# Kernel optimization log

Hardware: AMD Instinct MI355X
Metric: run time of the kernel (lower is better)

Reference implementation:

```python
import jax, jax.numpy as jnp
import numpy as np

N, E = 10000, 320000
IN_DIM = HID = OUT_DIM = 128
N_HEADS = 16
HEAD_DIM = OUT_DIM // N_HEADS  # 8
EDGE_FEAT_DIM, R_FEAT_DIM = 4, 64
KV_DIM = 2 * IN_DIM + EDGE_FEAT_DIM + R_FEAT_DIM  # 324
LN_EPS = 1e-5


def _layer_norm(x, g, b):
    mu = x.mean(-1, keepdims=True)
    var = ((x - mu) ** 2).mean(-1, keepdims=True)
    return (x - mu) / jnp.sqrt(var + LN_EPS) * g + b


def _mlp(x, W1, b1, g1, be1, W2, b2):
    # Linear -> LayerNorm -> ReLU -> Linear (2-layer MLP with norm=True)
    return jax.nn.relu(_layer_norm(x @ W1 + b1, g1, be1)) @ W2 + b2


def _mlp_params(key, din, dh, dout):
    k1, k2 = jax.random.split(key)
    return (jax.random.normal(k1, (din, dh), jnp.float32) / np.sqrt(din),
            jnp.zeros((dh,), jnp.float32),
            jnp.ones((dh,), jnp.float32),
            jnp.zeros((dh,), jnp.float32),
            jax.random.normal(k2, (dh, dout), jnp.float32) / np.sqrt(dh),
            jnp.zeros((dout,), jnp.float32))


def setup_inputs() -> dict:
    key = jax.random.key(0)
    ks = jax.random.split(key, 9)
    inp = {
        "h": jax.random.normal(ks[0], (N, IN_DIM), jnp.float32),
        "r_feat": jax.random.normal(ks[1], (E, R_FEAT_DIM), jnp.float32),
        "edge_feat": jax.random.normal(ks[2], (E, EDGE_FEAT_DIM), jnp.float32),
        "edge_index": jax.random.randint(ks[3], (2, E), 0, N, jnp.int32),
    }
    for name, (din, dout), k in [("hk", (KV_DIM, OUT_DIM), ks[4]),
                                 ("hv", (KV_DIM, OUT_DIM), ks[5]),
                                 ("hq", (IN_DIM, OUT_DIM), ks[6]),
                                 ("no", (2 * HID, HID), ks[7])]:
        W1, b1, g1, be1, W2, b2 = _mlp_params(k, din, HID, dout)
        inp.update({f"{name}_W1": W1, f"{name}_b1": b1, f"{name}_g1": g1,
                    f"{name}_be1": be1, f"{name}_W2": W2, f"{name}_b2": b2})
    inp["ew_W"] = jax.random.normal(ks[8], (R_FEAT_DIM, 1), jnp.float32) / np.sqrt(R_FEAT_DIM)
    inp["ew_b"] = jnp.zeros((1,), jnp.float32)
    return inp


def reference(h, r_feat, edge_feat, edge_index,
              hk_W1, hk_b1, hk_g1, hk_be1, hk_W2, hk_b2,
              hv_W1, hv_b1, hv_g1, hv_be1, hv_W2, hv_b2,
              hq_W1, hq_b1, hq_g1, hq_be1, hq_W2, hq_b2,
              no_W1, no_b1, no_g1, no_be1, no_W2, no_b2,
              ew_W, ew_b):
    src, dst = edge_index[0], edge_index[1]
    hi, hj = h[dst], h[src]  # [E, IN_DIM] gathers
    # kv_input = cat([edge_feat, r_feat, hi, hj])  (edge_feat prepended)
    kv_input = jnp.concatenate([edge_feat, r_feat, hi, hj], axis=-1)  # [E, KV_DIM]

    k = _mlp(kv_input, hk_W1, hk_b1, hk_g1, hk_be1, hk_W2, hk_b2).reshape(E, N_HEADS, HEAD_DIM)
    v = _mlp(kv_input, hv_W1, hv_b1, hv_g1, hv_be1, hv_W2, hv_b2)  # [E, OUT_DIM]
    e_w = jax.nn.sigmoid(r_feat @ ew_W + ew_b)  # [E, 1] (ew_net_type == 'r')
    v = (v * e_w).reshape(E, N_HEADS, HEAD_DIM)
    q = _mlp(h, hq_W1, hq_b1, hq_g1, hq_be1, hq_W2, hq_b2).reshape(N, N_HEADS, HEAD_DIM)

    # scatter_softmax over edges grouped by dst, per head
    logits = (q[dst] * k).sum(-1) / np.sqrt(HEAD_DIM)  # [E, N_HEADS]
    seg_max = jax.ops.segment_max(logits, dst, num_segments=N)
    ex = jnp.exp(logits - seg_max[dst])
    den = jax.ops.segment_sum(ex, dst, num_segments=N)
    alpha = ex / (den[dst] + 1e-16)  # [E, N_HEADS]

    msg = alpha[..., None] * v  # [E, N_HEADS, HEAD_DIM]
    out = jax.ops.segment_sum(msg, dst, num_segments=N).reshape(N, OUT_DIM)
    out = _mlp(jnp.concatenate([out, h], axis=-1), no_W1, no_b1, no_g1, no_be1, no_W2, no_b2)
    return out + h
```

## Files before the change

kernel.cpp:

```cpp
#include <hip/hip_runtime.h>
#include <hip/hip_bf16.h>

#define N_NODES 10000
#define N_EDGES 320000

typedef __attribute__((ext_vector_type(8))) short bf16x8;
typedef __attribute__((ext_vector_type(4))) float f32x4;

__device__ inline short f2bf(float x) {
    __hip_bfloat16 h = __float2bfloat16(x);
    union { __hip_bfloat16 h; short s; } u; u.h = h; return u.s;
}

__device__ inline void st_bf4(short* p, float4 v) {
    union { short s[4]; int2 i; } u;
    u.s[0] = f2bf(v.x); u.s[1] = f2bf(v.y); u.s[2] = f2bf(v.z); u.s[3] = f2bf(v.w);
    *(int2*)p = u.i;
}

__device__ inline void block_reduce4(float4& v, float4* red) {
    #pragma unroll
    for (int o = 32; o > 0; o >>= 1) {
        v.x += __shfl_down(v.x, o, 64);
        v.y += __shfl_down(v.y, o, 64);
        v.z += __shfl_down(v.z, o, 64);
        v.w += __shfl_down(v.w, o, 64);
    }
    __syncthreads();
    if ((threadIdx.x & 63) == 0) red[threadIdx.x >> 6] = v;
    __syncthreads();
    float4 a = red[0], b = red[1];
    v.x = a.x + b.x; v.y = a.y + b.y; v.z = a.z + b.z; v.w = a.w + b.w;
}

__global__ __launch_bounds__(256) void prep_wt_kernel(
    const float* __restrict__ Wk, const float* __restrict__ Wv,
    short* __restrict__ Wt, int K)
{
    int col = threadIdx.x, ch = blockIdx.x;
    const float* W = (col < 128) ? Wk : Wv;
    int c = col & 127;
    short tmp[32];
    #pragma unroll
    for (int kk = 0; kk < 32; ++kk) {
        int k = ch * 32 + kk;
        float w = (k < K) ? W[k * 128 + c] : 0.f;
        tmp[kk] = f2bf(w);
    }
    short* outp = Wt + ((size_t)ch * 256 + col) * 32;
    #pragma unroll
    for (int i = 0; i < 4; ++i) {
        union { short s[8]; int4 v; } u;
        #pragma unroll
        for (int j = 0; j < 8; ++j) u.s[j] = tmp[i * 8 + j];
        *(int4*)(outp + i * 8) = u.v;
    }
}

__global__ __launch_bounds__(256) void hist_kernel(
    const int* __restrict__ edge_index, int* __restrict__ cnt)
{
    int stride = gridDim.x * blockDim.x;
    for (int e = blockIdx.x * blockDim.x + threadIdx.x; e < N_EDGES; e += stride)
        atomicAdd(&cnt[edge_index[N_EDGES + e]], 1);
}

__global__ __launch_bounds__(256) void scan_kernel(
    const int* __restrict__ cnt, int* __restrict__ base, int* __restrict__ cursor)
{
    __shared__ int part[256];
    int t = threadIdx.x;
    int lo = t * 40, hi = min(lo + 40, N_NODES);
    int s = 0;
    for (int i = lo; i < hi; ++i) s += cnt[i];
    part[t] = s;
    __syncthreads();
    if (t == 0) {
        int run = 0;
        for (int i = 0; i < 256; ++i) { int v = part[i]; part[i] = run; run += v; }
    }
    __syncthreads();
    int run = part[t];
    for (int i = lo; i < hi; ++i) {
        base[i] = run; cursor[i] = run; run += cnt[i];
    }
}

__global__ __launch_bounds__(256) void scatter_ids_kernel(
    const int* __restrict__ edge_index, int* __restrict__ cursor,
    int* __restrict__ sorted)
{
    int stride = gridDim.x * blockDim.x;
    for (int e = blockIdx.x * blockDim.x + threadIdx.x; e < N_EDGES; e += stride) {
        int d = edge_index[N_EDGES + e];
        int pos = atomicAdd(&cursor[d], 1);
        sorted[pos] = e;
    }
}

__global__ __launch_bounds__(128) void q_kernel(
    const float* __restrict__ h,
    const float* __restrict__ W1, const float* __restrict__ b1,
    const float* __restrict__ g1, const float* __restrict__ be1,
    const float* __restrict__ W2, const float* __restrict__ b2,
    float* __restrict__ qout)
{
    __shared__ __align__(16) float x[128];
    __shared__ __align__(16) float r[128];
    __shared__ float4 red4[2];
    int n = blockIdx.x, tid = threadIdx.x;
    x[tid] = h[(long)n * 128 + tid];
    __syncthreads();
    float y = b1[tid];
    #pragma unroll 4
    for (int i4 = 0; i4 < 128; i4 += 4) {
        float4 c = *(const float4*)&x[i4];
        y = fmaf(c.x, W1[(i4 + 0) * 128 + tid], y);
        y = fmaf(c.y, W1[(i4 + 1) * 128 + tid], y);
        y = fmaf(c.z, W1[(i4 + 2) * 128 + tid], y);
        y = fmaf(c.w, W1[(i4 + 3) * 128 + tid], y);
    }
    float4 s = make_float4(y, y * y, 0.f, 0.f);
    block_reduce4(s, red4);
    float mu  = s.x * 0.0078125f;
    float var = s.y * 0.0078125f - mu * mu;
    float ny = (y - mu) * rsqrtf(var + 1e-5f) * g1[tid] + be1[tid];
    r[tid] = fmaxf(ny, 0.f);
    __syncthreads();
    float y2 = b2[tid];
    #pragma unroll 4
    for (int i4 = 0; i4 < 128; i4 += 4) {
        float4 c = *(const float4*)&r[i4];
        y2 = fmaf(c.x, W2[(i4 + 0) * 128 + tid], y2);
        y2 = fmaf(c.y, W2[(i4 + 1) * 128 + tid], y2);
        y2 = fmaf(c.z, W2[(i4 + 2) * 128 + tid], y2);
        y2 = fmaf(c.w, W2[(i4 + 3) * 128 + tid], y2);
    }
    qout[(long)n * 128 + tid] = y2;
}

__global__ __launch_bounds__(256, 3) void edge_kernel(
    const float* __restrict__ h, const float* __restrict__ r_feat,
    const float* __restrict__ edge_feat, const int* __restrict__ edge_index,
    const short* __restrict__ Wt1, const short* __restrict__ Wt2,
    const float* __restrict__ kb1, const float* __restrict__ kg1,
    const float* __restrict__ kbe1, const float* __restrict__ kb2,
    const float* __restrict__ vb1, const float* __restrict__ vg1,
    const float* __restrict__ vbe1, const float* __restrict__ vb2,
    const float* __restrict__ ewW, const float* __restrict__ ewb,
    const float* __restrict__ q,
    float* __restrict__ logits_g, short* __restrict__ voutS)
{
    __shared__ __align__(16) char smem[53760];
    short* A1   = (short*)smem;
    short* A2   = (short*)smem;
    short* vbuf = (short*)smem;
    float* qbuf = (float*)(smem + 17408);
    float* ln_s = (float*)(smem + 51200);
    float* ln_q = (float*)(smem + 52224);
    float* ew_s = (float*)(smem + 53248);
    int*   dst_s= (int*)(smem + 53504);

    const int tid  = threadIdx.x;
    const int w    = tid >> 6;
    const int lane = tid & 63;
    const int g    = lane >> 4;
    const int lr   = lane & 15;
    const int cw   = w * 64;
    const long eg0 = (long)blockIdx.x * 64;

    {
        int row = tid >> 2;
        int c4  = tid & 3;
        long eg = eg0 + row;
        int srcn = edge_index[eg];
        int dstn = edge_index[N_EDGES + eg];
        if (c4 == 0) dst_s[row] = dstn;
        short* arow = A1 + row * 360;
        if (c4 == 0) {
            float4 v = *(const float4*)&edge_feat[eg * 4];
            st_bf4(arow, v);
        }
        #pragma unroll
        for (int j = 0; j < 4; ++j) {
            float4 v = *(const float4*)&r_feat[eg * 64 + c4 * 16 + j * 4];
            st_bf4(arow + 4 + c4 * 16 + j * 4, v);
        }
        #pragma unroll
        for (int j = 0; j < 8; ++j) {
            float4 v = *(const float4*)&h[(size_t)dstn * 128 + c4 * 32 + j * 4];
            st_bf4(arow + 68 + c4 * 32 + j * 4, v);
        }
        #pragma unroll
        for (int j = 0; j < 8; ++j) {
            float4 v = *(const float4*)&h[(size_t)srcn * 128 + c4 * 32 + j * 4];
            st_bf4(arow + 196 + c4 * 32 + j * 4, v);
        }
        for (int gi = c4; gi < 9; gi += 4)
            *(int2*)(arow + 324 + gi * 4) = make_int2(0, 0);

        float p = 0.f;
        #pragma unroll
        for (int j = 0; j < 4; ++j) {
            float4 rv = *(const float4*)&r_feat[eg * 64 + c4 * 16 + j * 4];
            float4 wv = *(const float4*)&ewW[c4 * 16 + j * 4];
            p += rv.x * wv.x + rv.y * wv.y + rv.z * wv.z + rv.w * wv.w;
        }
        p += __shfl_xor(p, 1);
        p += __shfl_xor(p, 2);
        if (c4 == 0) ew_s[row] = 1.f / (1.f + expf(-(p + ewb[0])));
    }
    __syncthreads();

    f32x4 acc[4][4];
    const f32x4 zero4 = {0.f, 0.f, 0.f, 0.f};
    #pragma unroll
    for (int mf = 0; mf < 4; ++mf)
        #pragma unroll
        for (int nf = 0; nf < 4; ++nf) acc[mf][nf] = zero4;

    #pragma unroll 2
    for (int ks = 0; ks < 11; ++ks) {
        bf16x8 bfr[4], afr[4];
        const short* wb = Wt1 + (size_t)ks * 8192 + (cw + lr) * 32 + g * 8;
        #pragma unroll
        for (int nf = 0; nf < 4; ++nf)
            bfr[nf] = *(const bf16x8*)(wb + nf * 512);
        #pragma unroll
        for (int mf = 0; mf < 4; ++mf)
            afr[mf] = *(const bf16x8*)&A1[(mf * 16 + lr) * 360 + ks * 32 + g * 8];
        #pragma unroll
        for (int mf = 0; mf < 4; ++mf)
            #pragma unroll
            for (int nf = 0; nf < 4; ++nf)
                acc[mf][nf] = __builtin_amdgcn_mfma_f32_16x16x32_bf16(
                    afr[mf], bfr[nf], acc[mf][nf], 0, 0, 0);
    }

    const float* b1p  = (w < 2) ? kb1  : vb1;
    const float* g1p  = (w < 2) ? kg1  : vg1;
    const float* be1p = (w < 2) ? kbe1 : vbe1;
    const float* b2p  = (w < 2) ? kb2  : vb2;
    const int colm0 = cw & 127;
    float b1c[4], g1c[4], be1c[4], b2c[4];
    #pragma unroll
    for (int nf = 0; nf < 4; ++nf) {
        int cm = colm0 + nf * 16 + lr;
        b1c[nf] = b1p[cm]; g1c[nf] = g1p[cm]; be1c[nf] = be1p[cm]; b2c[nf] = b2p[cm];
    }
    float sum_[4][4], sq_[4][4];
    #pragma unroll
    for (int mf = 0; mf < 4; ++mf)
        #pragma unroll
        for (int r = 0; r < 4; ++r) { sum_[mf][r] = 0.f; sq_[mf][r] = 0.f; }
    #pragma unroll
    for (int mf = 0; mf < 4; ++mf)
        #pragma unroll
        for (int nf = 0; nf < 4; ++nf)
            #pragma unroll
            for (int r = 0; r < 4; ++r) {
                float a = acc[mf][nf][r] + b1c[nf];
                acc[mf][nf][r] = a;
                sum_[mf][r] += a;
                sq_[mf][r]  += a * a;
            }
    #pragma unroll
    for (int mf = 0; mf < 4; ++mf)
        #pragma unroll
        for (int r = 0; r < 4; ++r) {
            float s = sum_[mf][r], qq = sq_[mf][r];
            #pragma unroll
            for (int m = 1; m < 16; m <<= 1) {
                s  += __shfl_xor(s, m);
                qq += __shfl_xor(qq, m);
            }
            sum_[mf][r] = s; sq_[mf][r] = qq;
        }
    if (lr == 0) {
        #pragma unroll
        for (int mf = 0; mf < 4; ++mf)
            #pragma unroll
            for (int r = 0; r < 4; ++r) {
                int row = mf * 16 + g * 4 + r;
                ln_s[w * 64 + row] = sum_[mf][r];
                ln_q[w * 64 + row] = sq_[mf][r];
            }
    }
    __syncthreads();
    #pragma unroll
    for (int mf = 0; mf < 4; ++mf)
        #pragma unroll
        for (int r = 0; r < 4; ++r) {
            int row = mf * 16 + g * 4 + r;
            float mu  = (ln_s[w * 64 + row] + ln_s[(w ^ 1) * 64 + row]) * 0.0078125f;
            float ex2 = (ln_q[w * 64 + row] + ln_q[(w ^ 1) * 64 + row]) * 0.0078125f;
            float rs = rsqrtf(ex2 - mu * mu + 1e-5f);
            #pragma unroll
            for (int nf = 0; nf < 4; ++nf) {
                float nv = fmaxf((acc[mf][nf][r] - mu) * rs * g1c[nf] + be1c[nf], 0.f);
                A2[row * 264 + cw + nf * 16 + lr] = f2bf(nv);
            }
        }
    __syncthreads();

    #pragma unroll
    for (int mf = 0; mf < 4; ++mf)
        #pragma unroll
        for (int nf = 0; nf < 4; ++nf) acc[mf][nf] = zero4;
    const int kbase = (w < 2) ? 0 : 128;
    #pragma unroll 2
    for (int ks = 0; ks < 4; ++ks) {
        bf16x8 bfr[4], afr[4];
        const short* wb = Wt2 + (size_t)ks * 8192 + (cw + lr) * 32 + g * 8;
        #pragma unroll
        for (int nf = 0; nf < 4; ++nf)
            bfr[nf] = *(const bf16x8*)(wb + nf * 512);
        #pragma unroll
        for (int mf = 0; mf < 4; ++mf)
            afr[mf] = *(const bf16x8*)&A2[(mf * 16 + lr) * 264 + kbase + ks * 32 + g * 8];
        #pragma unroll
        for (int mf = 0; mf < 4; ++mf)
            #pragma unroll
            for (int nf = 0; nf < 4; ++nf)
                acc[mf][nf] = __builtin_amdgcn_mfma_f32_16x16x32_bf16(
                    afr[mf], bfr[nf], acc[mf][nf], 0, 0, 0);
    }
    __syncthreads();

    {
        int row = tid >> 2, c4 = tid & 3;
        int dstn = dst_s[row];
        #pragma unroll
        for (int j = 0; j < 8; ++j)
            *(float4*)&qbuf[row * 132 + c4 * 32 + j * 4] =
                *(const float4*)&q[(size_t)dstn * 128 + c4 * 32 + j * 4];
    }
    if (w >= 2) {
        #pragma unroll
        for (int mf = 0; mf < 4; ++mf)
            #pragma unroll
            for (int r = 0; r < 4; ++r) {
                int row = mf * 16 + g * 4 + r;
                float ew = ew_s[row];
                #pragma unroll
                for (int nf = 0; nf < 4; ++nf) {
                    float vv = (acc[mf][nf][r] + b2c[nf]) * ew;
                    vbuf[row * 136 + (cw - 128) + nf * 16 + lr] = f2bf(vv);
                }
            }
    }
    __syncthreads();

    if (w < 2) {
        #pragma unroll
        for (int mf = 0; mf < 4; ++mf)
            #pragma unroll
            for (int nf = 0; nf < 4; ++nf)
                #pragma unroll
                for (int r = 0; r < 4; ++r) {
                    int row = mf * 16 + g * 4 + r;
                    int col = cw + nf * 16 + lr;
                    float k2 = acc[mf][nf][r] + b2c[nf];
                    float p = k2 * qbuf[row * 132 + col];
                    p += __shfl_xor(p, 1);
                    p += __shfl_xor(p, 2);
                    p += __shfl_xor(p, 4);
                    if ((lane & 7) == 0) {
                        int head = col >> 3;
                        long eg = eg0 + row;
                        logits_g[eg * 16 + head] = p * 0.35355339059327373f;
                    }
                }
    }
    #pragma unroll
    for (int i = tid; i < 1024; i += 256) {
        int row = i >> 4, p8 = i & 15;
        *(int4*)&voutS[(eg0 + row) * 128 + p8 * 8] = *(const int4*)&vbuf[row * 136 + p8 * 8];
    }
}

__global__ __launch_bounds__(128) void gather_kernel(
    const int* __restrict__ base, const int* __restrict__ cnt,
    const int* __restrict__ sorted,
    const float* __restrict__ logits, const __hip_bfloat16* __restrict__ vout,
    float* __restrict__ msg)
{
    int d = blockIdx.x, t = threadIdx.x;
    int hd = t >> 3;
    int s = base[d], c = cnt[d];

    float m = -3.402823466e+38f;
    for (int i = (t & 7); i < c; i += 8) {
        int e = sorted[s + i];
        m = fmaxf(m, logits[(long)e * 16 + hd]);
    }
    m = fmaxf(m, __shfl_xor(m, 1));
    m = fmaxf(m, __shfl_xor(m, 2));
    m = fmaxf(m, __shfl_xor(m, 4));

    float acc = 0.f, den = 0.f;
    for (int i = 0; i < c; ++i) {
        int e = sorted[s + i];
        float ex = expf(logits[(long)e * 16 + hd] - m);
        den += ex;
        acc += ex * __bfloat162float(vout[(long)e * 128 + t]);
    }
    msg[(long)d * 128 + t] = acc / (den + 1e-16f);
}

__global__ __launch_bounds__(128) void out_kernel(
    const float* __restrict__ h, const float* __restrict__ msg,
    const float* __restrict__ W1, const float* __restrict__ b1,
    const float* __restrict__ g1, const float* __restrict__ be1,
    const float* __restrict__ W2, const float* __restrict__ b2,
    float* __restrict__ out)
{
    __shared__ __align__(16) float xin[256];
    __shared__ __align__(16) float r[128];
    __shared__ float4 red4[2];
    int n = blockIdx.x, tid = threadIdx.x;
    float hval = h[(long)n * 128 + tid];
    xin[tid] = msg[(long)n * 128 + tid];
    xin[128 + tid] = hval;
    __syncthreads();
    float y = b1[tid];
    #pragma unroll 4
    for (int i4 = 0; i4 < 256; i4 += 4) {
        float4 c = *(const float4*)&xin[i4];
        y = fmaf(c.x, W1[(i4 + 0) * 128 + tid], y);
        y = fmaf(c.y, W1[(i4 + 1) * 128 + tid], y);
        y = fmaf(c.z, W1[(i4 + 2) * 128 + tid], y);
        y = fmaf(c.w, W1[(i4 + 3) * 128 + tid], y);
    }
    float4 s = make_float4(y, y * y, 0.f, 0.f);
    block_reduce4(s, red4);
    float mu  = s.x * 0.0078125f;
    float var = s.y * 0.0078125f - mu * mu;
    float ny = (y - mu) * rsqrtf(var + 1e-5f) * g1[tid] + be1[tid];
    r[tid] = fmaxf(ny, 0.f);
    __syncthreads();
    float y2 = b2[tid];
    #pragma unroll 4
    for (int i4 = 0; i4 < 128; i4 += 4) {
        float4 c = *(const float4*)&r[i4];
        y2 = fmaf(c.x, W2[(i4 + 0) * 128 + tid], y2);
        y2 = fmaf(c.y, W2[(i4 + 1) * 128 + tid], y2);
        y2 = fmaf(c.z, W2[(i4 + 2) * 128 + tid], y2);
        y2 = fmaf(c.w, W2[(i4 + 3) * 128 + tid], y2);
    }
    out[(long)n * 128 + tid] = y2 + hval;
}

extern "C" void kernel_launch(void* const* d_in, const int* in_sizes, int n_in,
                              void* d_out, int out_size, void* d_ws, size_t ws_size,
                              hipStream_t stream) {
    (void)in_sizes; (void)n_in; (void)out_size; (void)ws_size;
    const float* h         = (const float*)d_in[0];
    const float* r_feat    = (const float*)d_in[1];
    const float* edge_feat = (const float*)d_in[2];
    const int*   edge_index= (const int*)d_in[3];
    const float* kW1 = (const float*)d_in[4],  *kb1 = (const float*)d_in[5];
    const float* kg1 = (const float*)d_in[6],  *kbe1= (const float*)d_in[7];
    const float* kW2 = (const float*)d_in[8],  *kb2 = (const float*)d_in[9];
    const float* vW1 = (const float*)d_in[10], *vb1 = (const float*)d_in[11];
    const float* vg1 = (const float*)d_in[12], *vbe1= (const float*)d_in[13];
    const float* vW2 = (const float*)d_in[14], *vb2 = (const float*)d_in[15];
    const float* qW1 = (const float*)d_in[16], *qb1 = (const float*)d_in[17];
    const float* qg1 = (const float*)d_in[18], *qbe1= (const float*)d_in[19];
    const float* qW2 = (const float*)d_in[20], *qb2 = (const float*)d_in[21];
    const float* oW1 = (const float*)d_in[22], *ob1 = (const float*)d_in[23];
    const float* og1 = (const float*)d_in[24], *obe1= (const float*)d_in[25];
    const float* oW2 = (const float*)d_in[26], *ob2 = (const float*)d_in[27];
    const float* ewW = (const float*)d_in[28], *ewb = (const float*)d_in[29];
    float* out = (float*)d_out;

    char* ws = (char*)d_ws;
    float* q      = (float*)(ws);
    float* msg    = (float*)(ws);
    float* logits = (float*)(ws + 5120000);
    short* voutS  = (short*)(ws + 25600000);
    short* Wt1    = (short*)(ws + 107520000);
    short* Wt2    = (short*)(ws + 107700224);
    int*   cnt    = (int*)(ws + 107765760);
    int*   base   = (int*)(ws + 107805760);
    int*   cursor = (int*)(ws + 107845760);
    int*   sorted = (int*)(ws + 107885760);

    hipMemsetAsync(cnt, 0, N_NODES * 4, stream);

    hist_kernel<<<1250, 256, 0, stream>>>(edge_index, cnt);
    scan_kernel<<<1, 256, 0, stream>>>(cnt, base, cursor);
    scatter_ids_kernel<<<1250, 256, 0, stream>>>(edge_index, cursor, sorted);

    prep_wt_kernel<<<11, 256, 0, stream>>>(kW1, vW1, Wt1, 324);
    prep_wt_kernel<<<4, 256, 0, stream>>>(kW2, vW2, Wt2, 128);

    q_kernel<<<N_NODES, 128, 0, stream>>>(h, qW1, qb1, qg1, qbe1, qW2, qb2, q);

    edge_kernel<<<N_EDGES / 64, 256, 0, stream>>>(
        h, r_feat, edge_feat, edge_index, Wt1, Wt2,
        kb1, kg1, kbe1, kb2, vb1, vg1, vbe1, vb2,
        ewW, ewb, q, logits, voutS);

    gather_kernel<<<N_NODES, 128, 0, stream>>>(base, cnt, sorted, logits,
        (const __hip_bfloat16*)voutS, msg);

    out_kernel<<<N_NODES, 128, 0, stream>>>(h, msg, oW1, ob1, og1, obe1, oW2, ob2, out);
}
```

Measured before the change: 656.2 us.

## Batch 8 nodes per block in node MLPs, shrink edge smem, cache edge ids

The q and out MLP kernels now process 8 nodes per block, so each weight load from global memory is reused across 8 rows instead of one. This cuts weight traffic and block count, at the cost of more registers and fewer, larger blocks. The edge kernel's shared-memory layout is compacted by overlaying the LayerNorm scratch onto the q buffer region, with an extra barrier added to keep that overlay safe. This lowers per-block LDS use and may allow higher occupancy. The gather kernel stages up to 512 sorted edge ids in shared memory and unrolls the accumulation loop, so each id is not re-read from global memory by every thread.

```diff
diff --git a/kernel.cpp b/kernel.cpp
--- a/kernel.cpp
+++ b/kernel.cpp
@@ -105,38 +105,61 @@
     const float* __restrict__ W2, const float* __restrict__ b2,
     float* __restrict__ qout)
 {
-    __shared__ __align__(16) float x[128];
-    __shared__ __align__(16) float r[128];
+    __shared__ __align__(16) float xs[8][128];
+    __shared__ __align__(16) float rs[8][128];
     __shared__ float4 red4[2];
-    int n = blockIdx.x, tid = threadIdx.x;
-    x[tid] = h[(long)n * 128 + tid];
-    __syncthreads();
-    float y = b1[tid];
-    #pragma unroll 4
+    int n0 = blockIdx.x * 8, tid = threadIdx.x;
+    #pragma unroll
+    for (int n = 0; n < 8; ++n)
+        xs[n][tid] = h[(long)(n0 + n) * 128 + tid];
+    __syncthreads();
+    float y[8];
+    {
+        float b = b1[tid];
+        #pragma unroll
+        for (int n = 0; n < 8; ++n) y[n] = b;
+    }
     for (int i4 = 0; i4 < 128; i4 += 4) {
-        float4 c = *(const float4*)&x[i4];
-        y = fmaf(c.x, W1[(i4 + 0) * 128 + tid], y);
-        y = fmaf(c.y, W1[(i4 + 1) * 128 + tid], y);
-        y = fmaf(c.z, W1[(i4 + 2) * 128 + tid], y);
-        y = fmaf(c.w, W1[(i4 + 3) * 128 + tid], y);
-    }
-    float4 s = make_float4(y, y * y, 0.f, 0.f);
-    block_reduce4(s, red4);
-    float mu  = s.x * 0.0078125f;
-    float var = s.y * 0.0078125f - mu * mu;
-    float ny = (y - mu) * rsqrtf(var + 1e-5f) * g1[tid] + be1[tid];
-    r[tid] = fmaxf(ny, 0.f);
-    __syncthreads();
-    float y2 = b2[tid];
-    #pragma unroll 4
+        float w0 = W1[(i4 + 0) * 128 + tid], w1 = W1[(i4 + 1) * 128 + tid];
+        float w2 = W1[(i4 + 2) * 128 + tid], w3 = W1[(i4 + 3) * 128 + tid];
+        #pragma unroll
+        for (int n = 0; n < 8; ++n) {
+            float4 c = *(const float4*)&xs[n][i4];
+            y[n] = fmaf(c.x, w0, y[n]); y[n] = fmaf(c.y, w1, y[n]);
+            y[n] = fmaf(c.z, w2, y[n]); y[n] = fmaf(c.w, w3, y[n]);
+        }
+    }
+    float gv = g1[tid], bev = be1[tid];
+    #pragma unroll 1
+    for (int p = 0; p < 4; ++p) {
+        int na = 2 * p, nb = 2 * p + 1;
+        float4 s = make_float4(y[na], y[na] * y[na], y[nb], y[nb] * y[nb]);
+        block_reduce4(s, red4);
+        float muA = s.x * 0.0078125f, vA = s.y * 0.0078125f - muA * muA;
+        float muB = s.z * 0.0078125f, vB = s.w * 0.0078125f - muB * muB;
+        rs[na][tid] = fmaxf((y[na] - muA) * rsqrtf(vA + 1e-5f) * gv + bev, 0.f);
+        rs[nb][tid] = fmaxf((y[nb] - muB) * rsqrtf(vB + 1e-5f) * gv + bev, 0.f);
+    }
+    __syncthreads();
+    float y2[8];
+    {
+        float b = b2[tid];
+        #pragma unroll
+        for (int n = 0; n < 8; ++n) y2[n] = b;
+    }
     for (int i4 = 0; i4 < 128; i4 += 4) {
-        float4 c = *(const float4*)&r[i4];
-        y2 = fmaf(c.x, W2[(i4 + 0) * 128 + tid], y2);
-        y2 = fmaf(c.y, W2[(i4 + 1) * 128 + tid], y2);
-        y2 = fmaf(c.z, W2[(i4 + 2) * 128 + tid], y2);
-        y2 = fmaf(c.w, W2[(i4 + 3) * 128 + tid], y2);
-    }
-    qout[(long)n * 128 + tid] = y2;
+        float w0 = W2[(i4 + 0) * 128 + tid], w1 = W2[(i4 + 1) * 128 + tid];
+        float w2 = W2[(i4 + 2) * 128 + tid], w3 = W2[(i4 + 3) * 128 + tid];
+        #pragma unroll
+        for (int n = 0; n < 8; ++n) {
+            float4 c = *(const float4*)&rs[n][i4];
+            y2[n] = fmaf(c.x, w0, y2[n]); y2[n] = fmaf(c.y, w1, y2[n]);
+            y2[n] = fmaf(c.z, w2, y2[n]); y2[n] = fmaf(c.w, w3, y2[n]);
+        }
+    }
+    #pragma unroll
+    for (int n = 0; n < 8; ++n)
+        qout[(long)(n0 + n) * 128 + tid] = y2[n];
 }
 
 __global__ __launch_bounds__(256, 3) void edge_kernel(
@@ -151,15 +174,15 @@
     const float* __restrict__ q,
     float* __restrict__ logits_g, short* __restrict__ voutS)
 {
-    __shared__ __align__(16) char smem[53760];
+    __shared__ __align__(16) char smem[51712];
     short* A1   = (short*)smem;
     short* A2   = (short*)smem;
     short* vbuf = (short*)smem;
     float* qbuf = (float*)(smem + 17408);
-    float* ln_s = (float*)(smem + 51200);
-    float* ln_q = (float*)(smem + 52224);
-    float* ew_s = (float*)(smem + 53248);
-    int*   dst_s= (int*)(smem + 53504);
+    float* ln_s = (float*)(smem + 33792);
+    float* ln_q = (float*)(smem + 34816);
+    float* ew_s = (float*)(smem + 51200);
+    int*   dst_s= (int*)(smem + 51456);
 
     const int tid  = threadIdx.x;
     const int w    = tid >> 6;
@@ -276,6 +299,7 @@
             }
             sum_[mf][r] = s; sq_[mf][r] = qq;
         }
+    __syncthreads();
     if (lr == 0) {
         #pragma unroll
         for (int mf = 0; mf < 4; ++mf)
@@ -385,13 +409,17 @@
     const float* __restrict__ logits, const __hip_bfloat16* __restrict__ vout,
     float* __restrict__ msg)
 {
+    __shared__ int eids[512];
     int d = blockIdx.x, t = threadIdx.x;
     int hd = t >> 3;
     int s = base[d], c = cnt[d];
 
+    for (int i = t; i < c && i < 512; i += 128) eids[i] = sorted[s + i];
+    __syncthreads();
+
     float m = -3.402823466e+38f;
     for (int i = (t & 7); i < c; i += 8) {
-        int e = sorted[s + i];
+        int e = (i < 512) ? eids[i] : sorted[s + i];
         m = fmaxf(m, logits[(long)e * 16 + hd]);
     }
     m = fmaxf(m, __shfl_xor(m, 1));
@@ -399,8 +427,9 @@
     m = fmaxf(m, __shfl_xor(m, 4));
 
     float acc = 0.f, den = 0.f;
+    #pragma unroll 2
     for (int i = 0; i < c; ++i) {
-        int e = sorted[s + i];
+        int e = (i < 512) ? eids[i] : sorted[s + i];
         float ex = expf(logits[(long)e * 16 + hd] - m);
         den += ex;
         acc += ex * __bfloat162float(vout[(long)e * 128 + t]);
@@ -415,40 +444,65 @@
     const float* __restrict__ W2, const float* __restrict__ b2,
     float* __restrict__ out)
 {
-    __shared__ __align__(16) float xin[256];
-    __shared__ __align__(16) float r[128];
+    __shared__ __align__(16) float xin[8][256];
+    __shared__ __align__(16) float rbuf[8][128];
     __shared__ float4 red4[2];
-    int n = blockIdx.x, tid = threadIdx.x;
-    float hval = h[(long)n * 128 + tid];
-    xin[tid] = msg[(long)n * 128 + tid];
-    xin[128 + tid] = hval;
-    __syncthreads();
-    float y = b1[tid];
-    #pragma unroll 4
+    int n0 = blockIdx.x * 8, tid = threadIdx.x;
+    float hv[8];
+    #pragma unroll
+    for (int n = 0; n < 8; ++n) {
+        hv[n] = h[(long)(n0 + n) * 128 + tid];
+        xin[n][tid] = msg[(long)(n0 + n) * 128 + tid];
+        xin[n][128 + tid] = hv[n];
+    }
+    __syncthreads();
+    float y[8];
+    {
+        float b = b1[tid];
+        #pragma unroll
+        for (int n = 0; n < 8; ++n) y[n] = b;
+    }
     for (int i4 = 0; i4 < 256; i4 += 4) {
-        float4 c = *(const float4*)&xin[i4];
-        y = fmaf(c.x, W1[(i4 + 0) * 128 + tid], y);
-        y = fmaf(c.y, W1[(i4 + 1) * 128 + tid], y);
-        y = fmaf(c.z, W1[(i4 + 2) * 128 + tid], y);
-        y = fmaf(c.w, W1[(i4 + 3) * 128 + tid], y);
-    }
-    float4 s = make_float4(y, y * y, 0.f, 0.f);
-    block_reduce4(s, red4);
-    float mu  = s.x * 0.0078125f;
-    float var = s.y * 0.0078125f - mu * mu;
-    float ny = (y - mu) * rsqrtf(var + 1e-5f) * g1[tid] + be1[tid];
-    r[tid] = fmaxf(ny, 0.f);
-    __syncthreads();
-    float y2 = b2[tid];
-    #pragma unroll 4
+        float w0 = W1[(i4 + 0) * 128 + tid], w1 = W1[(i4 + 1) * 128 + tid];
+        float w2 = W1[(i4 + 2) * 128 + tid], w3 = W1[(i4 + 3) * 128 + tid];
+        #pragma unroll
+        for (int n = 0; n < 8; ++n) {
+            float4 c = *(const float4*)&xin[n][i4];
+            y[n] = fmaf(c.x, w0, y[n]); y[n] = fmaf(c.y, w1, y[n]);
+            y[n] = fmaf(c.z, w2, y[n]); y[n] = fmaf(c.w, w3, y[n]);
+        }
+    }
+    float gv = g1[tid], bev = be1[tid];
+    #pragma unroll 1
+    for (int p = 0; p < 4; ++p) {
+        int na = 2 * p, nb = 2 * p + 1;
+        float4 s = make_float4(y[na], y[na] * y[na], y[nb], y[nb] * y[nb]);
+        block_reduce4(s, red4);
+        float muA = s.x * 0.0078125f, vA = s.y * 0.0078125f - muA * muA;
+        float muB = s.z * 0.0078125f, vB = s.w * 0.0078125f - muB * muB;
+        rbuf[na][tid] = fmaxf((y[na] - muA) * rsqrtf(vA + 1e-5f) * gv + bev, 0.f);
+        rbuf[nb][tid] = fmaxf((y[nb] - muB) * rsqrtf(vB + 1e-5f) * gv + bev, 0.f);
+    }
+    __syncthreads();
+    float y2[8];
+    {
+        float b = b2[tid];
+        #pragma unroll
+        for (int n = 0; n < 8; ++n) y2[n] = b;
+    }
     for (int i4 = 0; i4 < 128; i4 += 4) {
-        float4 c = *(const float4*)&r[i4];
-        y2 = fmaf(c.x, W2[(i4 + 0) * 128 + tid], y2);
-        y2 = fmaf(c.y, W2[(i4 + 1) * 128 + tid], y2);
-        y2 = fmaf(c.z, W2[(i4 + 2) * 128 + tid], y2);
-        y2 = fmaf(c.w, W2[(i4 + 3) * 128 + tid], y2);
-    }
-    out[(long)n * 128 + tid] = y2 + hval;
+        float w0 = W2[(i4 + 0) * 128 + tid], w1 = W2[(i4 + 1) * 128 + tid];
+        float w2 = W2[(i4 + 2) * 128 + tid], w3 = W2[(i4 + 3) * 128 + tid];
+        #pragma unroll
+        for (int n = 0; n < 8; ++n) {
+            float4 c = *(const float4*)&rbuf[n][i4];
+            y2[n] = fmaf(c.x, w0, y2[n]); y2[n] = fmaf(c.y, w1, y2[n]);
+            y2[n] = fmaf(c.z, w2, y2[n]); y2[n] = fmaf(c.w, w3, y2[n]);
+        }
+    }
+    #pragma unroll
+    for (int n = 0; n < 8; ++n)
+        out[(long)(n0 + n) * 128 + tid] = y2[n] + hv[n];
 }
 
 extern "C" void kernel_launch(void* const* d_in, const int* in_sizes, int n_in,
@@ -495,7 +549,7 @@
     prep_wt_kernel<<<11, 256, 0, stream>>>(kW1, vW1, Wt1, 324);
     prep_wt_kernel<<<4, 256, 0, stream>>>(kW2, vW2, Wt2, 128);
 
-    q_kernel<<<N_NODES, 128, 0, stream>>>(h, qW1, qb1, qg1, qbe1, qW2, qb2, q);
+    q_kernel<<<N_NODES / 8, 128, 0, stream>>>(h, qW1, qb1, qg1, qbe1, qW2, qb2, q);
 
     edge_kernel<<<N_EDGES / 64, 256, 0, stream>>>(
         h, r_feat, edge_feat, edge_index, Wt1, Wt2,
@@ -505,5 +559,5 @@
     gather_kernel<<<N_NODES, 128, 0, stream>>>(base, cnt, sorted, logits,
         (const __hip_bfloat16*)voutS, msg);
 
-    out_kernel<<<N_NODES, 128, 0, stream>>>(h, msg, oW1, ob1, og1, obe1, oW2, ob2, out);
-}
+    out_kernel<<<N_NODES / 8, 128, 0, stream>>>(h, msg, oW1, ob1, og1, obe1, oW2, ob2, out);
+}
```

Result: faster. 598.7 us (-8.8%).
